# Performance work log

Hardware: AMD Instinct MI355X
Metric: run time of the kernel (lower is better)

## Reference

```python
import jax, jax.numpy as jnp
import numpy as np

GROUP = 128

def _dequant(q, s, z):
    # q: [O, K] int4 values in [0,16); s,z: [O, K//GROUP]
    O, K = q.shape
    qg = q.reshape(O, K // GROUP, GROUP)
    w = (qg - z[:, :, None]).astype(s.dtype) * s[:, :, None]
    return w.reshape(O, K)

def setup_inputs() -> dict:
    key = jax.random.key(0)
    ks = jax.random.split(key, 7)
    H, I = 4096, 14336
    x = jax.random.normal(ks[0], (2, 2048, H), jnp.float32)
    q_up = jax.random.randint(ks[1], (I, H), 0, 16, jnp.int32)
    s_up = (jax.random.uniform(ks[2], (I, H // GROUP), jnp.float32) * 0.02 + 1e-3)
    z_up = jax.random.randint(ks[3], (I, H // GROUP), 0, 16, jnp.int32)
    q_down = jax.random.randint(ks[4], (H, I), 0, 16, jnp.int32)
    s_down = (jax.random.uniform(ks[5], (H, I // GROUP), jnp.float32) * 0.02 + 1e-3)
    z_down = jax.random.randint(ks[6], (H, I // GROUP), 0, 16, jnp.int32)
    return {"x": x, "q_up": q_up, "s_up": s_up, "z_up": z_up,
            "q_down": q_down, "s_down": s_down, "z_down": z_down}

def reference(x, q_up, s_up, z_up, q_down, s_down, z_down):
    # up_proj: W4A16 dequant + GEMM, weight layout [out, in] like nn.Linear
    w_up = _dequant(q_up, s_up, z_up)        # [I, H]
    h = jnp.einsum('bsh,ih->bsi', x, w_up)   # [B, S, I]
    # NemotronH 'relu2' activation: relu(h)^2
    a = jnp.square(jax.nn.relu(h))
    w_down = _dequant(q_down, s_down, z_down)  # [H, I]
    y = jnp.einsum('bsi,hi->bsh', a, w_down)   # [B, S, H]
    return y
```

## Files before the change

kernel.cpp:

```cpp
#include <hip/hip_runtime.h>
#include <stdint.h>

typedef unsigned short u16;
typedef __attribute__((ext_vector_type(4))) float f32x4;
typedef __attribute__((ext_vector_type(8))) __bf16 bf16x8;
typedef __attribute__((ext_vector_type(8))) unsigned short u16x8;

__device__ __forceinline__ u16 f2bf(float f) {
  unsigned u = __builtin_bit_cast(unsigned, f);
  u = (u + 0x7fffu + ((u >> 16) & 1u)) >> 16;
  return (u16)u;
}

typedef __attribute__((address_space(1))) const void gvoid_t;
typedef __attribute__((address_space(3))) void lvoid_t;

__device__ __forceinline__ void gload_lds16(const void* g, void* l) {
  __builtin_amdgcn_global_load_lds((gvoid_t*)g, (lvoid_t*)l, 16, 0, 0);
}

__global__ __launch_bounds__(256)
void dequant_kernel(const int* __restrict__ q, const float* __restrict__ s,
                    const int* __restrict__ z, u16* __restrict__ w, int K) {
  const int row = blockIdx.y;
  const int k = (blockIdx.x * 256 + threadIdx.x) << 3;
  const int ng = K >> 7;
  const int g = k >> 7;
  const float sv = s[(size_t)row * ng + g];
  const float zv = (float)z[(size_t)row * ng + g];
  const int4* qp = (const int4*)(q + (size_t)row * K + k);
  const int4 a = qp[0], b = qp[1];
  u16x8 o;
  o[0] = f2bf(((float)a.x - zv) * sv);
  o[1] = f2bf(((float)a.y - zv) * sv);
  o[2] = f2bf(((float)a.z - zv) * sv);
  o[3] = f2bf(((float)a.w - zv) * sv);
  o[4] = f2bf(((float)b.x - zv) * sv);
  o[5] = f2bf(((float)b.y - zv) * sv);
  o[6] = f2bf(((float)b.z - zv) * sv);
  o[7] = f2bf(((float)b.w - zv) * sv);
  *reinterpret_cast<u16x8*>(w + (size_t)row * K + k) = o;
}

__global__ __launch_bounds__(256)
void cvt_kernel(const float* __restrict__ in, u16* __restrict__ out) {
  const size_t i = ((size_t)blockIdx.x * 256 + threadIdx.x) << 3;
  const float4* p = (const float4*)(in + i);
  const float4 a = p[0], b = p[1];
  u16x8 o;
  o[0] = f2bf(a.x); o[1] = f2bf(a.y); o[2] = f2bf(a.z); o[3] = f2bf(a.w);
  o[4] = f2bf(b.x); o[5] = f2bf(b.y); o[6] = f2bf(b.z); o[7] = f2bf(b.w);
  *reinterpret_cast<u16x8*>(out + i) = o;
}

template<bool RELU2>
__global__ __launch_bounds__(512, 2)
void gemm256(const u16* __restrict__ Ap, const u16* __restrict__ Bp,
             void* __restrict__ Cptr, int M, int N, int K) {
  __shared__ __align__(16) u16 As[2][256][64];
  __shared__ __align__(16) u16 Bs[2][256][64];
  const int tid = threadIdx.x;
  const int lane = tid & 63;
  const int wid = tid >> 6;
  const int wr = wid >> 2, wc = wid & 3;

  const int nbx = N >> 8;
  const int nwg = gridDim.x;
  int bid = blockIdx.x;
  bid = (bid & 7) * (nwg >> 3) + (bid >> 3);
  const int m0 = (bid / nbx) << 8;
  const int n0 = (bid % nbx) << 8;

  const int srow = tid >> 3;
  const int scol = tid & 7;
  const int lr = lane & 15;
  const int lk = (lane >> 4) << 3;
  const int xorc = (lr & 7) << 3;

  const char* baA0 = (const char*)&As[0][0][0] + (wr * 128 + lr) * 128;
  const char* baA1 = baA0 + 32768;
  const char* baB0 = (const char*)&Bs[0][0][0] + (wc * 64 + lr) * 128;
  const char* baB1 = baB0 + 32768;
  const int koff0 = (lk ^ xorc) * 2;

  f32x4 acc[8][4] = {};
  bf16x8 a1[4], a2[4], a3[4], a4[4], b1[4], b2[4];

  const int nk = K >> 6;

#define STG_A(bufi, h, kt) do { _Pragma("unroll") \
  for (int l_ = 0; l_ < 2; ++l_) { \
    const int r_ = (h) * 128 + l_ * 64 + srow; \
    gload_lds16(Ap + (size_t)(m0 + r_) * K + (size_t)((kt) << 6) + ((scol ^ (srow & 7)) << 3), \
                &As[bufi][r_][scol << 3]); } } while (0)
#define STG_B(bufi, h, kt) do { _Pragma("unroll") \
  for (int l_ = 0; l_ < 2; ++l_) { \
    const int r_ = (h) * 128 + l_ * 64 + srow; \
    gload_lds16(Bp + (size_t)(n0 + r_) * K + (size_t)((kt) << 6) + ((scol ^ (srow & 7)) << 3), \
                &Bs[bufi][r_][scol << 3]); } } while (0)
#define RD_A(base, ks, half, dst) do { _Pragma("unroll") \
  for (int i_ = 0; i_ < 4; ++i_) \
    dst[i_] = *reinterpret_cast<const bf16x8*>( \
      (base) + ((half) * 4 + i_) * 2048 + (koff0 ^ ((ks) * 64))); } while (0)
#define RD_B(base, ks, dst) do { _Pragma("unroll") \
  for (int j_ = 0; j_ < 4; ++j_) \
    dst[j_] = *reinterpret_cast<const bf16x8*>( \
      (base) + j_ * 2048 + (koff0 ^ ((ks) * 64))); } while (0)
#define MFMA16(ASET, BSET, I0) do { _Pragma("unroll") \
  for (int i_ = 0; i_ < 4; ++i_) { _Pragma("unroll") \
    for (int j_ = 0; j_ < 4; ++j_) \
      acc[(I0) + i_][j_] = __builtin_amdgcn_mfma_f32_16x16x32_bf16( \
        ASET[i_], BSET[j_], acc[(I0) + i_][j_], 0, 0, 0); } } while (0)
#define BARO() do { asm volatile("" ::: "memory"); __builtin_amdgcn_s_barrier(); \
  asm volatile("" ::: "memory"); } while (0)
#define LGKM(n) do { asm volatile("s_waitcnt lgkmcnt(" #n ")" ::: "memory"); \
  __builtin_amdgcn_sched_barrier(0); } while (0)
#define SB0 __builtin_amdgcn_sched_barrier(0)
#define GATE4 asm volatile("s_waitcnt vmcnt(4)" ::: "memory")
#define PRIO(Q) do { __builtin_amdgcn_s_setprio(1); Q; __builtin_amdgcn_s_setprio(0); } while (0)
#define TILE4(bA, bB, SA1, SA2, SB3, SB4) do { \
  BARO(); \
  RD_B(bB, 0, b1); RD_A(bA, 0, 0, a1); \
  LGKM(0); \
  SA1; \
  PRIO(MFMA16(a1, b1, 0)); \
  SB0; RD_B(bB, 1, b2); SB0; RD_A(bA, 0, 1, a2); SB0; RD_A(bA, 1, 1, a4); SB0; RD_A(bA, 1, 0, a3); \
  BARO(); \
  LGKM(8); \
  SA2; \
  PRIO(MFMA16(a2, b1, 4)); \
  BARO(); \
  LGKM(4); \
  SB3; \
  PRIO(MFMA16(a4, b2, 4)); \
  BARO(); \
  LGKM(0); \
  SB4; \
  PRIO(MFMA16(a3, b2, 0)); \
  GATE4; \
} while (0)

  STG_A(0, 0, 0); STG_A(0, 1, 0);
  STG_B(0, 0, 0); STG_B(0, 1, 0);
  STG_B(1, 0, 1); STG_B(1, 1, 1);
  asm volatile("s_waitcnt vmcnt(4)" ::: "memory");

  const int nit = nk >> 1;
  for (int it = 0; it < nit; ++it) {
    const int t1 = 2 * it + 1;
    int t2 = 2 * it + 2; if (t2 >= nk) t2 -= nk;
    int t3 = 2 * it + 3; if (t3 >= nk) t3 -= nk;
    TILE4(baA0, baB0, STG_A(1, 0, t1), STG_A(1, 1, t1), STG_B(0, 0, t2), STG_B(0, 1, t2));
    TILE4(baA1, baB1, STG_A(0, 0, t2), STG_A(0, 1, t2), STG_B(1, 0, t3), STG_B(1, 1, t3));
  }
  asm volatile("s_waitcnt vmcnt(0)" ::: "memory");

  const int crow = (lane >> 4) << 2;
  const int ccol = lane & 15;
#pragma unroll
  for (int i = 0; i < 8; ++i) {
#pragma unroll
    for (int j = 0; j < 4; ++j) {
#pragma unroll
      for (int q = 0; q < 4; ++q) {
        const int m = m0 + wr * 128 + i * 16 + crow + q;
        const int n = n0 + wc * 64 + j * 16 + ccol;
        const float v = acc[i][j][q];
        if constexpr (RELU2) {
          const float r = fmaxf(v, 0.f);
          ((u16*)Cptr)[(size_t)m * N + n] = f2bf(r * r);
        } else {
          ((float*)Cptr)[(size_t)m * N + n] = v;
        }
      }
    }
  }
#undef STG_A
#undef STG_B
#undef RD_A
#undef RD_B
#undef MFMA16
#undef BARO
#undef LGKM
#undef SB0
#undef GATE4
#undef PRIO
#undef TILE4
}

extern "C" void kernel_launch(void* const* d_in, const int* in_sizes, int n_in,
                              void* d_out, int out_size, void* d_ws, size_t ws_size,
                              hipStream_t stream) {
  const float* x    = (const float*)d_in[0];
  const int*   q_up = (const int*)d_in[1];
  const float* s_up = (const float*)d_in[2];
  const int*   z_up = (const int*)d_in[3];
  const int*   q_dn = (const int*)d_in[4];
  const float* s_dn = (const float*)d_in[5];
  const int*   z_dn = (const int*)d_in[6];
  float* y = (float*)d_out;

  const int H = 4096, I = 14336;
  const int M = in_sizes[0] / H;

  const size_t wbytes = (size_t)I * H * 2;
  const size_t abytes = (size_t)M * I * 2;
  const size_t xbytes = (size_t)M * H * 2;
  u16* wbuf = (u16*)d_ws;
  u16* abuf = (u16*)((char*)d_ws + wbytes);
  u16* xbf  = (u16*)((char*)d_ws + wbytes + abytes);
  if (ws_size < wbytes + abytes + xbytes) return;

  dequant_kernel<<<dim3(H / 8 / 256, I), 256, 0, stream>>>(q_up, s_up, z_up, wbuf, H);
  cvt_kernel<<<dim3((int)(((size_t)M * H) >> 11)), 256, 0, stream>>>(x, xbf);
  gemm256<true><<<dim3((M / 256) * (I / 256)), 512, 0, stream>>>(xbf, wbuf, abuf, M, I, H);
  dequant_kernel<<<dim3(I / 8 / 256, H), 256, 0, stream>>>(q_dn, s_dn, z_dn, wbuf, I);
  gemm256<false><<<dim3((M / 256) * (H / 256)), 512, 0, stream>>>(abuf, wbuf, y, M, H, I);
}
```

Before: 952.3 us.

## Switch GEMM inner loop to 32x32x16 bf16 MFMA tiles

Replaces the 16x16x32 MFMA tiling with 32x32x16 MFMA instructions. Each wave now holds a 4x2 grid of 32x32 accumulators, and the LDS read pattern, swizzle offset and epilogue index mapping are rewritten to match. The larger MFMA raises math per LDS read and per instruction issue. In exchange it changes the register pressure and the LDS bank access pattern, and the wait counts in the software pipeline may no longer match the new number of reads.

```diff
diff --git a/kernel.cpp b/kernel.cpp
--- a/kernel.cpp
+++ b/kernel.cpp
@@ -2,7 +2,7 @@
 #include <stdint.h>
 
 typedef unsigned short u16;
-typedef __attribute__((ext_vector_type(4))) float f32x4;
+typedef __attribute__((ext_vector_type(16))) float f32x16;
 typedef __attribute__((ext_vector_type(8))) __bf16 bf16x8;
 typedef __attribute__((ext_vector_type(8))) unsigned short u16x8;
 
@@ -73,18 +73,16 @@
 
   const int srow = tid >> 3;
   const int scol = tid & 7;
-  const int lr = lane & 15;
-  const int lk = (lane >> 4) << 3;
-  const int xorc = (lr & 7) << 3;
-
-  const char* baA0 = (const char*)&As[0][0][0] + (wr * 128 + lr) * 128;
+  const int l31 = lane & 31;
+
+  const char* baA0 = (const char*)&As[0][0][0] + (wr * 128 + l31) * 128;
   const char* baA1 = baA0 + 32768;
-  const char* baB0 = (const char*)&Bs[0][0][0] + (wc * 64 + lr) * 128;
+  const char* baB0 = (const char*)&Bs[0][0][0] + (wc * 64 + l31) * 128;
   const char* baB1 = baB0 + 32768;
-  const int koff0 = (lk ^ xorc) * 2;
-
-  f32x4 acc[8][4] = {};
-  bf16x8 a1[4], a2[4], a3[4], a4[4], b1[4], b2[4];
+  const int koff0 = (((lane >> 5) ^ (lane & 7)) << 4);
+
+  f32x16 acc[4][2] = {};
+  bf16x8 a0[4], a1[4], a2[4], a3[4], b0[2], b1[2], b2[2], b3[2];
 
   const int nk = K >> 6;
 
@@ -98,19 +96,19 @@
     const int r_ = (h) * 128 + l_ * 64 + srow; \
     gload_lds16(Bp + (size_t)(n0 + r_) * K + (size_t)((kt) << 6) + ((scol ^ (srow & 7)) << 3), \
                 &Bs[bufi][r_][scol << 3]); } } while (0)
-#define RD_A(base, ks, half, dst) do { _Pragma("unroll") \
-  for (int i_ = 0; i_ < 4; ++i_) \
-    dst[i_] = *reinterpret_cast<const bf16x8*>( \
-      (base) + ((half) * 4 + i_) * 2048 + (koff0 ^ ((ks) * 64))); } while (0)
+#define RD_A(base, ks, dst) do { _Pragma("unroll") \
+  for (int f_ = 0; f_ < 4; ++f_) \
+    dst[f_] = *reinterpret_cast<const bf16x8*>( \
+      (base) + f_ * 4096 + (koff0 ^ ((ks) << 5))); } while (0)
 #define RD_B(base, ks, dst) do { _Pragma("unroll") \
-  for (int j_ = 0; j_ < 4; ++j_) \
-    dst[j_] = *reinterpret_cast<const bf16x8*>( \
-      (base) + j_ * 2048 + (koff0 ^ ((ks) * 64))); } while (0)
-#define MFMA16(ASET, BSET, I0) do { _Pragma("unroll") \
+  for (int f_ = 0; f_ < 2; ++f_) \
+    dst[f_] = *reinterpret_cast<const bf16x8*>( \
+      (base) + f_ * 4096 + (koff0 ^ ((ks) << 5))); } while (0)
+#define MFMA8(ASET, BSET) do { _Pragma("unroll") \
   for (int i_ = 0; i_ < 4; ++i_) { _Pragma("unroll") \
-    for (int j_ = 0; j_ < 4; ++j_) \
-      acc[(I0) + i_][j_] = __builtin_amdgcn_mfma_f32_16x16x32_bf16( \
-        ASET[i_], BSET[j_], acc[(I0) + i_][j_], 0, 0, 0); } } while (0)
+    for (int j_ = 0; j_ < 2; ++j_) \
+      acc[i_][j_] = __builtin_amdgcn_mfma_f32_32x32x16_bf16( \
+        ASET[i_], BSET[j_], acc[i_][j_], 0, 0, 0); } } while (0)
 #define BARO() do { asm volatile("" ::: "memory"); __builtin_amdgcn_s_barrier(); \
   asm volatile("" ::: "memory"); } while (0)
 #define LGKM(n) do { asm volatile("s_waitcnt lgkmcnt(" #n ")" ::: "memory"); \
@@ -120,23 +118,24 @@
 #define PRIO(Q) do { __builtin_amdgcn_s_setprio(1); Q; __builtin_amdgcn_s_setprio(0); } while (0)
 #define TILE4(bA, bB, SA1, SA2, SB3, SB4) do { \
   BARO(); \
-  RD_B(bB, 0, b1); RD_A(bA, 0, 0, a1); \
+  RD_B(bB, 0, b0); RD_A(bA, 0, a0); \
   LGKM(0); \
   SA1; \
-  PRIO(MFMA16(a1, b1, 0)); \
-  SB0; RD_B(bB, 1, b2); SB0; RD_A(bA, 0, 1, a2); SB0; RD_A(bA, 1, 1, a4); SB0; RD_A(bA, 1, 0, a3); \
+  PRIO(MFMA8(a0, b0)); \
+  SB0; RD_B(bB, 1, b1); SB0; RD_B(bB, 2, b2); SB0; RD_B(bB, 3, b3); \
+  SB0; RD_A(bA, 1, a1); SB0; RD_A(bA, 2, a2); SB0; RD_A(bA, 3, a3); \
   BARO(); \
   LGKM(8); \
   SA2; \
-  PRIO(MFMA16(a2, b1, 4)); \
+  PRIO(MFMA8(a1, b1)); \
   BARO(); \
   LGKM(4); \
   SB3; \
-  PRIO(MFMA16(a4, b2, 4)); \
+  PRIO(MFMA8(a2, b2)); \
   BARO(); \
   LGKM(0); \
   SB4; \
-  PRIO(MFMA16(a3, b2, 0)); \
+  PRIO(MFMA8(a3, b3)); \
   GATE4; \
 } while (0)
 
@@ -153,22 +152,21 @@
     TILE4(baA0, baB0, STG_A(1, 0, t1), STG_A(1, 1, t1), STG_B(0, 0, t2), STG_B(0, 1, t2));
     TILE4(baA1, baB1, STG_A(0, 0, t2), STG_A(0, 1, t2), STG_B(1, 0, t3), STG_B(1, 1, t3));
   }
-  asm volatile("s_waitcnt vmcnt(0)" ::: "memory");
-
-  const int crow = (lane >> 4) << 2;
-  const int ccol = lane & 15;
+  asm volatile("s_waitcnt vmcnt(0) lgkmcnt(0)" ::: "memory");
+
+  const int hi = lane >> 5;
 #pragma unroll
-  for (int i = 0; i < 8; ++i) {
+  for (int fi = 0; fi < 4; ++fi) {
 #pragma unroll
-    for (int j = 0; j < 4; ++j) {
+    for (int fj = 0; fj < 2; ++fj) {
 #pragma unroll
-      for (int q = 0; q < 4; ++q) {
-        const int m = m0 + wr * 128 + i * 16 + crow + q;
-        const int n = n0 + wc * 64 + j * 16 + ccol;
-        const float v = acc[i][j][q];
+      for (int r = 0; r < 16; ++r) {
+        const int m = m0 + wr * 128 + fi * 32 + (r & 3) + 8 * (r >> 2) + 4 * hi;
+        const int n = n0 + wc * 64 + fj * 32 + l31;
+        const float v = acc[fi][fj][r];
         if constexpr (RELU2) {
-          const float r = fmaxf(v, 0.f);
-          ((u16*)Cptr)[(size_t)m * N + n] = f2bf(r * r);
+          const float rr = fmaxf(v, 0.f);
+          ((u16*)Cptr)[(size_t)m * N + n] = f2bf(rr * rr);
         } else {
           ((float*)Cptr)[(size_t)m * N + n] = v;
         }
@@ -179,7 +177,7 @@
 #undef STG_B
 #undef RD_A
 #undef RD_B
-#undef MFMA16
+#undef MFMA8
 #undef BARO
 #undef LGKM
 #undef SB0
```

Measured after the change: 1.057 ms. +11.0%, slower.
